# Kernel optimization log

Measured on AMD Instinct MI355X. Metric: run time of the kernel, lower is better.

Reference implementation:

```python
import jax, jax.numpy as jnp
import numpy as np

B, T = 8, 32
D = 256                      # recurrent dim = 4*8*8 (product of embed dims)
SPEAKERS = 2
OUT_CELL = 64
N_CLASSES = 6
NUM_LAYERS = 2               # original shares ONE QRNNCell across layers ([cell]*num_layers)
BETA = 0.8                   # QActivation beta (scale_factor = 1)

def _unitary(rng, n):
    a = rng.normal(size=(n, n)) + 1j * rng.normal(size=(n, n))
    q, _ = np.linalg.qr(a)
    return jnp.asarray(q.real, jnp.float32), jnp.asarray(q.imag, jnp.float32)

def setup_inputs():
    key = jax.random.key(0)
    ks = jax.random.split(key, 18)
    rng = np.random.default_rng(0)
    def lin(k, fi, fo):
        kw, kb = jax.random.split(k)
        lim = 1.0 / np.sqrt(fi)
        return (jax.random.uniform(kw, (fi, fo), jnp.float32, -lim, lim),
                jax.random.uniform(kb, (fo,), jnp.float32, -lim, lim))
    Wt, bt = lin(ks[0], 300, 4)
    Wa, ba = lin(ks[1], 74, 8)
    Wv, bv = lin(ks[2], 35, 8)
    W1, b1 = lin(ks[3], D, OUT_CELL)
    W2, b2 = lin(ks[4], OUT_CELL, N_CLASSES)
    Ux_r, Ux_i = _unitary(rng, D)
    Uh_r, Uh_i = _unitary(rng, D)
    two_pi = float(2.0 * np.pi)
    return {
        'x_text': jax.random.normal(ks[5], (B, T, 300), jnp.float32),
        'x_audio': jax.random.normal(ks[6], (B, T, 74), jnp.float32),
        'x_video': jax.random.normal(ks[7], (B, T, 35), jnp.float32),
        'smask': jax.random.uniform(ks[8], (B, T, SPEAKERS), jnp.float32),
        'Wt': Wt, 'bt': bt, 'Wa': Wa, 'ba': ba, 'Wv': Wv, 'bv': bv,
        'Pt': jax.random.uniform(ks[9], (SPEAKERS, 4), jnp.float32, 0.0, two_pi),
        'Pa': jax.random.uniform(ks[10], (SPEAKERS, 8), jnp.float32, 0.0, two_pi),
        'Pv': jax.random.uniform(ks[11], (SPEAKERS, 8), jnp.float32, 0.0, two_pi),
        'Ux_r': Ux_r, 'Ux_i': Ux_i, 'Uh_r': Uh_r, 'Uh_i': Uh_i,
        'Lambda': jax.random.normal(ks[12], (), jnp.float32),
        'Kr': jax.random.normal(ks[13], (D, D), jnp.float32),
        'Ki': jax.random.normal(ks[14], (D, D), jnp.float32),
        'W1': W1, 'b1': b1, 'W2': W2, 'b2': b2,
    }

def _forward(x_text, x_audio, x_video, spk, Wt, bt, Wa, ba, Wv, bv, Pt, Pa, Pv,
             Ux_r, Ux_i, Uh_r, Uh_i, Lambda, Kr, Ki, W1, b1, W2, b2):
    def pure_state(x, W, b, P):
        r = jax.nn.relu(x @ W + b)
        amp = r / jnp.maximum(jnp.linalg.norm(r, axis=-1, keepdims=True), 1e-12)  # F.normalize
        ph = P[spk]                                   # (B,T,e) phase lookup by speaker id
        return amp * jnp.cos(ph), amp * jnp.sin(ph)   # ComplexMultiply
    tr_, ti_ = pure_state(x_text, Wt, bt, Pt)
    ar_, ai_ = pure_state(x_audio, Wa, ba, Pa)
    vr_, vi_ = pure_state(x_video, Wv, bv, Pv)
    def ckron(xr, xi, yr, yi):                        # QProduct: complex Kronecker product
        rr = jnp.einsum('bti,btj->btij', xr, yr) - jnp.einsum('bti,btj->btij', xi, yi)
        ii = jnp.einsum('bti,btj->btij', xr, yi) + jnp.einsum('bti,btj->btij', xi, yr)
        b_, t_ = rr.shape[:2]
        return rr.reshape(b_, t_, -1), ii.reshape(b_, t_, -1)
    pr, pi = ckron(tr_, ti_, ar_, ai_)
    pr, pi = ckron(pr, pi, vr_, vi_)                  # (B,T,D)
    # QOuter: rho = |psi><psi|, stored time-major for the scan
    rho_r = jnp.einsum('bti,btj->tbij', pr, pr) + jnp.einsum('bti,btj->tbij', pi, pi)
    rho_i = jnp.einsum('bti,btj->tbij', pi, pr) - jnp.einsum('bti,btj->tbij', pr, pi)
    lam = jax.nn.sigmoid(Lambda)
    eye = jnp.eye(D, dtype=pr.dtype) / D
    def evolve(Ur, Ui, rr, ri):                       # U rho U^dagger (complex, real/imag parts)
        Ar = jnp.einsum('pq,bqr->bpr', Ur, rr) - jnp.einsum('pq,bqr->bpr', Ui, ri)
        Ai = jnp.einsum('pq,bqr->bpr', Ur, ri) + jnp.einsum('pq,bqr->bpr', Ui, rr)
        Br = jnp.einsum('bpq,rq->bpr', Ar, Ur) + jnp.einsum('bpq,rq->bpr', Ai, Ui)
        Bi = jnp.einsum('bpq,rq->bpr', Ai, Ur) - jnp.einsum('bpq,rq->bpr', Ar, Ui)
        return Br, Bi
    def step(carry, x):                               # QRNNCell; activation only on emitted state
        hr, hi = carry
        xr, xi = x
        xer, xei = evolve(Ux_r, Ux_i, xr, xi)
        her, hei = evolve(Uh_r, Uh_i, hr, hi)
        nr = lam * xer + (1.0 - lam) * her
        ni = lam * xei + (1.0 - lam) * hei
        return (nr, ni), (BETA * nr + (1.0 - BETA) * eye, BETA * ni)  # QActivation (depolarize)
    xs = (rho_r, rho_i)
    for _ in range(NUM_LAYERS):                       # same (shared) cell each layer
        init = (jnp.broadcast_to(eye, rho_r.shape[1:]), jnp.zeros(rho_r.shape[1:], pr.dtype))
        _, xs = jax.lax.scan(step, init, xs)
    hr, hi = xs                                       # (T,B,D,D)
    # QMeasurement: p_k = Re <v_k| rho |v_k>, v_k L2-normalized complex vectors
    nrm = jnp.sqrt(jnp.sum(Kr * Kr + Ki * Ki, axis=-1, keepdims=True))
    mr, mi = Kr / nrm, Ki / nrm
    Prj_r = jnp.einsum('ki,kj->kij', mr, mr) + jnp.einsum('ki,kj->kij', mi, mi)
    Prj_i = jnp.einsum('ki,kj->kij', mr, mi) - jnp.einsum('ki,kj->kij', mi, mr)
    probs = jnp.einsum('tbij,kij->tbk', hr, Prj_r) - jnp.einsum('tbij,kij->tbk', hi, Prj_i)
    h1 = jax.nn.relu(probs @ W1 + b1)                 # SimpleNet (dropout = identity at eval)
    out = jnp.tanh(h1 @ W2 + b2)                      # (T,B,C)
    return jax.nn.log_softmax(jnp.moveaxis(out, 0, 1), axis=-1)  # (B,T,C)

def reference(x_text, x_audio, x_video, smask, Wt, bt, Wa, ba, Wv, bv, Pt, Pa, Pv,
              Ux_r, Ux_i, Uh_r, Uh_i, Lambda, Kr, Ki, W1, b1, W2, b2):
    spk = jnp.argmax(smask, axis=-1)
    return _forward(x_text, x_audio, x_video, spk, Wt, bt, Wa, ba, Wv, bv, Pt, Pa, Pv,
                    Ux_r, Ux_i, Uh_r, Uh_i, Lambda, Kr, Ki, W1, b1, W2, b2)
```

## Files before the change

kernel.cpp:

```cpp
#include <hip/hip_runtime.h>

#define TT 32
#define BETA_ 0.8f

typedef __bf16 bf16_t;
typedef bf16_t bf16x8 __attribute__((ext_vector_type(8)));
typedef float f32x4 __attribute__((ext_vector_type(4)));

#define PACC_F 256
#define BF_BASE_B 263168L
#define US4 262144L
#define XU  131072L
#define XIB_E (76L * US4)

__device__ inline f32x4 MF(bf16x8 a, bf16x8 b, f32x4 c) {
    return __builtin_amdgcn_mfma_f32_16x16x32_bf16(a, b, c, 0, 0, 0);
}

__device__ inline void splitW(float vr, float vi, bf16_t* o, long idx, int full) {
    bf16_t rh = (bf16_t)vr; o[idx] = rh;
    bf16_t ih = (bf16_t)vi; o[65536L + idx] = ih;
    if (full) {
        o[2 * 65536L + idx] = (bf16_t)(vr - (float)rh);
        o[3 * 65536L + idx] = (bf16_t)(vi - (float)ih);
    }
}

__global__ __launch_bounds__(256) void k_prep(
    const float* __restrict__ xt, const float* __restrict__ xa, const float* __restrict__ xv,
    const float* __restrict__ sm,
    const float* __restrict__ Wt, const float* __restrict__ bt,
    const float* __restrict__ Wa, const float* __restrict__ ba,
    const float* __restrict__ Wv, const float* __restrict__ bv,
    const float* __restrict__ Pt, const float* __restrict__ Pa, const float* __restrict__ Pv,
    const float* __restrict__ Uxr, const float* __restrict__ Uxi,
    const float* __restrict__ Uhr, const float* __restrict__ Uhi,
    const float* __restrict__ Lam, const float* __restrict__ Kr, const float* __restrict__ Ki,
    void* wsv)
{
    float* WF = (float*)wsv;
    bf16_t* bf = (bf16_t*)((char*)wsv + BF_BASE_B);
    const int blk = blockIdx.x, tid = threadIdx.x;
    __shared__ float red[256];
    __shared__ float rt[4], ra[8], rv[8], inv3[3];

    if (blk == 0) {
        if (tid != 0) return;
        float lam = 1.f / (1.f + expf(-Lam[0]));
        float oml = 1.f - lam;
        WF[0] = lam;
        WF[1] = BETA_ * BETA_ * lam * lam;
        float w = 1.f;
        for (int n = 0; n < 64; ++n) { WF[64 + n] = w; w *= oml; }
        float a1 = 1.f / 256.f, a2 = 1.f / 256.f;
        for (int t = 0; t < 32; ++t) {
            a1 = oml * a1;
            float y1 = BETA_ * a1 + (1.f - BETA_) / 256.f;
            a2 = lam * y1 + oml * a2;
            WF[8 + t] = BETA_ * a2 + (1.f - BETA_) / 256.f;
        }
        return;
    }
    if (blk < 513) {
        int i = (blk - 1) & 255, j = tid;
        if (blk < 257) {
            splitW(Uxr[i * 256 + j], Uxi[i * 256 + j], bf + 0 * US4, (long)i * 256 + j, 1);
        } else {
            float vr = Uhr[i * 256 + j], vi = Uhi[i * 256 + j];
            splitW(vr, vi, bf + 1 * US4, (long)i * 256 + j, 1);
            splitW(vr, vi, bf + 2 * US4, (long)j * 256 + i, 1);
        }
        return;
    }
    if (blk < 769) {
        const int colS = blk - 513;
        const int t0 = colS >> 3, b = colS & 7;
        const long bt_ = (long)b * TT + t0;
        if (tid < 4) {
            float acc = bt[tid];
            const float* x = xt + bt_ * 300;
            for (int q = 0; q < 300; ++q) acc = fmaf(x[q], Wt[q * 4 + tid], acc);
            rt[tid] = fmaxf(acc, 0.f);
        } else if (tid < 12) {
            int u = tid - 4;
            float acc = ba[u];
            const float* x = xa + bt_ * 74;
            for (int q = 0; q < 74; ++q) acc = fmaf(x[q], Wa[q * 8 + u], acc);
            ra[u] = fmaxf(acc, 0.f);
        } else if (tid < 20) {
            int u = tid - 12;
            float acc = bv[u];
            const float* x = xv + bt_ * 35;
            for (int q = 0; q < 35; ++q) acc = fmaf(x[q], Wv[q * 8 + u], acc);
            rv[u] = fmaxf(acc, 0.f);
        }
        __syncthreads();
        if (tid == 0) {
            float s = 0.f; for (int u = 0; u < 4; ++u) s += rt[u] * rt[u];
            inv3[0] = 1.f / fmaxf(sqrtf(s), 1e-12f);
            s = 0.f; for (int u = 0; u < 8; ++u) s += ra[u] * ra[u];
            inv3[1] = 1.f / fmaxf(sqrtf(s), 1e-12f);
            s = 0.f; for (int u = 0; u < 8; ++u) s += rv[u] * rv[u];
            inv3[2] = 1.f / fmaxf(sqrtf(s), 1e-12f);
        }
        __syncthreads();
        float s0 = sm[bt_ * 2], s1 = sm[bt_ * 2 + 1];
        int spk = (s1 > s0) ? 1 : 0;
        int d = tid;
        int ti = d >> 6, ai = (d >> 3) & 7, vi = d & 7;
        float amp = (rt[ti] * inv3[0]) * (ra[ai] * inv3[1]) * (rv[vi] * inv3[2]);
        float ph = Pt[spk * 4 + ti] + Pa[spk * 8 + ai] + Pv[spk * 8 + vi];
        splitW(amp * cosf(ph), amp * sinf(ph), bf + 3 * US4, (long)colS * 256 + d, 1);
        return;
    }
    if (blk < 1025) {
        int k = blk - 769, i = tid;
        float vr = Kr[k * 256 + i], vi = Ki[k * 256 + i];
        red[i] = vr * vr + vi * vi;
        __syncthreads();
        for (int s = 128; s > 0; s >>= 1) { if (i < s) red[i] += red[i + s]; __syncthreads(); }
        float inv = 1.f / sqrtf(red[0]);
        splitW(vr * inv, -vi * inv, bf + 44 * US4, (long)k * 256 + i, 1);
        return;
    }
    WF[PACC_F + (blk - 1025) * 256 + tid] = 0.f;
}

template<int LO, int WFull>
__device__ __forceinline__ void chain_body(const bf16_t* __restrict__ A,
                                           const bf16_t* __restrict__ B,
                                           bf16_t* __restrict__ C,
                                           int m0, int n0, int wm, int wn, int fr, int fg)
{
    constexpr int NP = LO ? 2 : 4;
    const bf16_t* Ab = A + (long)(m0 + wm * 32 + fr) * 256 + fg * 8;
    const bf16_t* Bb = B + (long)(n0 + wn * 32 + fr) * 256 + fg * 8;
    f32x4 rp[2][2] = {}, rn[2][2] = {}, im[2][2] = {};
    bf16x8 a0[2][NP], b0[2][NP], a1[2][NP], b1[2][NP];

#define CLD(abuf, bbuf, ks)                                                            \
    {                                                                                  \
        _Pragma("unroll") for (int fm = 0; fm < 2; ++fm)                               \
            _Pragma("unroll") for (int pl = 0; pl < NP; ++pl)                          \
                abuf[fm][pl] = *(const bf16x8*)(Ab + pl * 65536L + fm * 4096L + (ks) * 32); \
        _Pragma("unroll") for (int fn = 0; fn < 2; ++fn)                               \
            _Pragma("unroll") for (int pl = 0; pl < NP; ++pl)                          \
                bbuf[fn][pl] = *(const bf16x8*)(Bb + pl * 65536L + fn * 4096L + (ks) * 32); \
    }
#define CMM(abuf, bbuf)                                                                \
    {                                                                                  \
        _Pragma("unroll") for (int fm = 0; fm < 2; ++fm)                               \
            _Pragma("unroll") for (int fn = 0; fn < 2; ++fn) {                         \
                rp[fm][fn] = MF(abuf[fm][0], bbuf[fn][0], rp[fm][fn]);                 \
                rn[fm][fn] = MF(abuf[fm][1], bbuf[fn][1], rn[fm][fn]);                 \
                im[fm][fn] = MF(abuf[fm][0], bbuf[fn][1], im[fm][fn]);                 \
                im[fm][fn] = MF(abuf[fm][1], bbuf[fn][0], im[fm][fn]);                 \
                if (!LO) {                                                             \
                    rp[fm][fn] = MF(abuf[fm][0], bbuf[fn][2], rp[fm][fn]);             \
                    rp[fm][fn] = MF(abuf[fm][2], bbuf[fn][0], rp[fm][fn]);             \
                    rn[fm][fn] = MF(abuf[fm][1], bbuf[fn][3], rn[fm][fn]);             \
                    rn[fm][fn] = MF(abuf[fm][3], bbuf[fn][1], rn[fm][fn]);             \
                    im[fm][fn] = MF(abuf[fm][0], bbuf[fn][3], im[fm][fn]);             \
                    im[fm][fn] = MF(abuf[fm][2], bbuf[fn][1], im[fm][fn]);             \
                    im[fm][fn] = MF(abuf[fm][1], bbuf[fn][2], im[fm][fn]);             \
                    im[fm][fn] = MF(abuf[fm][3], bbuf[fn][0], im[fm][fn]);             \
                }                                                                      \
            }                                                                          \
    }
    CLD(a0, b0, 0);
    CLD(a1, b1, 1);
    CMM(a0, b0); CLD(a0, b0, 2);
    CMM(a1, b1); CLD(a1, b1, 3);
    CMM(a0, b0); CLD(a0, b0, 4);
    CMM(a1, b1); CLD(a1, b1, 5);
    CMM(a0, b0); CLD(a0, b0, 6);
    CMM(a1, b1); CLD(a1, b1, 7);
    CMM(a0, b0);
    CMM(a1, b1);
#undef CLD
#undef CMM
#pragma unroll
    for (int fm = 0; fm < 2; ++fm)
#pragma unroll
        for (int fn = 0; fn < 2; ++fn)
#pragma unroll
            for (int r4 = 0; r4 < 4; ++r4) {
                int m = m0 + wm * 32 + fm * 16 + fg * 4 + r4;
                int n = n0 + wn * 32 + fn * 16 + fr;
                float vr = rp[fm][fn][r4] - rn[fm][fn][r4];
                splitW(vr, im[fm][fn][r4], C, (long)m * 256 + n, WFull);
            }
}

struct Jobs {
    long aB[4], aS[4], bB[4], cB[4], cS[4];
    int cnt[4], lo[4], wf[4];
};

__global__ __launch_bounds__(256, 2) void k_chain(void* wsv, Jobs J)
{
    bf16_t* bf = (bf16_t*)((char*)wsv + BF_BASE_B);
    int z = blockIdx.y, j = 0;
    while (z >= J.cnt[j]) { z -= J.cnt[j]; ++j; }
    const bf16_t* A = bf + J.aB[j] + (long)z * J.aS[j];
    const bf16_t* B = bf + J.bB[j];
    bf16_t*       C = bf + J.cB[j] + (long)z * J.cS[j];
    const int m0 = (blockIdx.x & 3) * 64, n0 = (blockIdx.x >> 2) * 64;
    const int tid = threadIdx.x, lane = tid & 63, w = tid >> 6;
    const int wm = w >> 1, wn = w & 1, fr = lane & 15, fg = lane >> 4;
    if (J.lo[j])      chain_body<1, 0>(A, B, C, m0, n0, wm, wn, fr, fg);
    else if (J.wf[j]) chain_body<0, 1>(A, B, C, m0, n0, wm, wn, fr, fg);
    else              chain_body<0, 0>(A, B, C, m0, n0, wm, wn, fr, fg);
}

struct MJ { int pref[33]; };

__global__ __launch_bounds__(256, 3) void k_measure7(void* wsv, MJ J)
{
    float* WF = (float*)wsv;
    bf16_t* bf = (bf16_t*)((char*)wsv + BF_BASE_B);
    int bid = blockIdx.x;
    int t = 0;
    while (bid >= J.pref[t + 1]) ++t;
    int jid = bid - J.pref[t];
    const int kblk = jid & 3;
    int g = jid >> 2;
    int c = 0;
    for (;;) { int cnt2 = ((t - c) >> 3) + 1; if (g < cnt2) break; g -= cnt2; ++c; }
    const int colc = g;
    const int k0 = kblk * 64;

    const int tid = threadIdx.x, lane = tid & 63, w = tid >> 6;
    const int wm = w >> 1, wn = w & 1;
    const int fr = lane & 15, fg = lane >> 4;
    __shared__ float part[64][9];

    int g2_[2], t0_[2], val_[2];
    const bf16_t* Bb_[2];
#pragma unroll
    for (int fn = 0; fn < 2; ++fn) {
        g2_[fn] = colc * 64 + wn * 32 + fn * 16 + fr;
        t0_[fn] = g2_[fn] >> 3;
        int av = t - c - t0_[fn];
        val_[fn] = (av >= 0);
        Bb_[fn] = bf + XIB_E + (long)(val_[fn] ? av : 0) * XU + (long)g2_[fn] * 256 + fg * 8;
    }
    const bf16_t* Ab = bf + (44L + c) * US4 + (long)(k0 + wm * 32 + fr) * 256 + fg * 8;

    f32x4 rp[2][2] = {}, rn[2][2] = {}, im[2][2] = {};
    bf16x8 a0[2][2], b0[2][2], a1[2][2], b1[2][2];

#define MLD(abuf, bbuf, ks)                                                            \
    {                                                                                  \
        _Pragma("unroll") for (int fm = 0; fm < 2; ++fm)                               \
            _Pragma("unroll") for (int pl = 0; pl < 2; ++pl)                           \
                abuf[fm][pl] = *(const bf16x8*)(Ab + pl * 65536L + fm * 4096L + (ks) * 32); \
        _Pragma("unroll") for (int fn = 0; fn < 2; ++fn)                               \
            _Pragma("unroll") for (int pl = 0; pl < 2; ++pl) {                         \
                bf16x8 v = bf16x8{};                                                   \
                if (val_[fn]) v = *(const bf16x8*)(Bb_[fn] + pl * 65536L + (ks) * 32); \
                bbuf[fn][pl] = v;                                                      \
            }                                                                          \
    }
#define MMM(abuf, bbuf)                                                                \
    {                                                                                  \
        _Pragma("unroll") for (int fm = 0; fm < 2; ++fm)                               \
            _Pragma("unroll") for (int fn = 0; fn < 2; ++fn) {                         \
                rp[fm][fn] = MF(abuf[fm][0], bbuf[fn][0], rp[fm][fn]);                 \
                rn[fm][fn] = MF(abuf[fm][1], bbuf[fn][1], rn[fm][fn]);                 \
                im[fm][fn] = MF(abuf[fm][0], bbuf[fn][1], im[fm][fn]);                 \
                im[fm][fn] = MF(abuf[fm][1], bbuf[fn][0], im[fm][fn]);                 \
            }                                                                          \
    }
    MLD(a0, b0, 0);
    MLD(a1, b1, 1);
    MMM(a0, b0); MLD(a0, b0, 2);
    MMM(a1, b1); MLD(a1, b1, 3);
    MMM(a0, b0); MLD(a0, b0, 4);
    MMM(a1, b1); MLD(a1, b1, 5);
    MMM(a0, b0); MLD(a0, b0, 6);
    MMM(a1, b1); MLD(a1, b1, 7);
    MMM(a0, b0);
    MMM(a1, b1);
#undef MLD
#undef MMM

    for (int e = tid; e < 64 * 9; e += 256) (&part[0][0])[e] = 0.f;
    __syncthreads();
#pragma unroll
    for (int fm = 0; fm < 2; ++fm)
#pragma unroll
        for (int fn = 0; fn < 2; ++fn)
#pragma unroll
            for (int r4 = 0; r4 < 4; ++r4) {
                float vr = rp[fm][fn][r4] - rn[fm][fn][r4];
                float vi = im[fm][fn][r4];
                float v = vr * vr + vi * vi;
                int kl = wm * 32 + fm * 16 + fg * 4 + r4;
                if (val_[fn] && t0_[fn] <= t)
                    atomicAdd(&part[kl][g2_[fn] & 7], WF[64 + t - t0_[fn]] * v);
            }
    __syncthreads();
    float* pacc = WF + PACC_F;
    for (int e = tid; e < 512; e += 256) {
        int kl = e >> 3, b = e & 7;
        float v = part[kl][b];
        if (v != 0.f) atomicAdd(&pacc[((t * 8 + b) << 8) + k0 + kl], v);
    }
}

__global__ __launch_bounds__(64) void k_mlp(
    const float* __restrict__ W1, const float* __restrict__ b1,
    const float* __restrict__ W2, const float* __restrict__ b2,
    const float* __restrict__ WF, float* __restrict__ out)
{
    const int t = blockIdx.x >> 3, b = blockIdx.x & 7;
    const int tid = threadIdx.x;
    __shared__ float pp[256], hh[64], oo[6];
    float ft = WF[8 + t], s2 = WF[1];
    const float* pacc = WF + PACC_F + ((t * 8 + b) << 8);
    for (int k = tid; k < 256; k += 64) pp[k] = ft + s2 * pacc[k];
    __syncthreads();
    float acc = b1[tid];
    for (int k = 0; k < 256; ++k) acc = fmaf(pp[k], W1[k * 64 + tid], acc);
    hh[tid] = fmaxf(acc, 0.f);
    __syncthreads();
    if (tid < 6) {
        float a = b2[tid];
        for (int k = 0; k < 64; ++k) a = fmaf(hh[k], W2[k * 6 + tid], a);
        oo[tid] = tanhf(a);
    }
    __syncthreads();
    if (tid == 0) {
        float m = oo[0];
        for (int c2 = 1; c2 < 6; ++c2) m = fmaxf(m, oo[c2]);
        float s = 0.f;
        for (int c2 = 0; c2 < 6; ++c2) s += expf(oo[c2] - m);
        float lse = m + logf(s);
        for (int c2 = 0; c2 < 6; ++c2) out[((long)b * 32 + t) * 6 + c2] = oo[c2] - lse;
    }
}

static inline void setJob(Jobs& J, int i, long aB, long aS, long bB, long cB, long cS,
                          int cnt, int lo, int wf)
{
    J.aB[i] = aB; J.aS[i] = aS; J.bB[i] = bB; J.cB[i] = cB; J.cS[i] = cS;
    J.cnt[i] = cnt; J.lo[i] = lo; J.wf[i] = wf;
}

extern "C" void kernel_launch(void* const* d_in, const int* in_sizes, int n_in,
                              void* d_out, int out_size, void* d_ws, size_t ws_size,
                              hipStream_t stream)
{
    const float* xt  = (const float*)d_in[0];
    const float* xa  = (const float*)d_in[1];
    const float* xv  = (const float*)d_in[2];
    const float* sm  = (const float*)d_in[3];
    const float* Wt  = (const float*)d_in[4];
    const float* bt  = (const float*)d_in[5];
    const float* Wa  = (const float*)d_in[6];
    const float* ba  = (const float*)d_in[7];
    const float* Wv  = (const float*)d_in[8];
    const float* bv  = (const float*)d_in[9];
    const float* Pt  = (const float*)d_in[10];
    const float* Pa  = (const float*)d_in[11];
    const float* Pv  = (const float*)d_in[12];
    const float* Uxr = (const float*)d_in[13];
    const float* Uxi = (const float*)d_in[14];
    const float* Uhr = (const float*)d_in[15];
    const float* Uhi = (const float*)d_in[16];
    const float* Lam = (const float*)d_in[17];
    const float* Kr  = (const float*)d_in[18];
    const float* Ki  = (const float*)d_in[19];
    const float* W1  = (const float*)d_in[20];
    const float* b1  = (const float*)d_in[21];
    const float* W2  = (const float*)d_in[22];
    const float* b2  = (const float*)d_in[23];
    float* WF  = (float*)d_ws;
    float* out = (float*)d_out;

    k_prep<<<1281, 256, 0, stream>>>(xt, xa, xv, sm, Wt, bt, Wa, ba, Wv, bv,
                                     Pt, Pa, Pv, Uxr, Uxi, Uhr, Uhi, Lam, Kr, Ki, d_ws);

    auto U = [](int u) { return (long)u * US4; };
    dim3 blk(256);
    Jobs J;

    setJob(J, 0, U(1), 0, U(2), U(4), 0, 1, 0, 1);
    setJob(J, 1, U(2), 0, U(1), U(5), 0, 1, 0, 1);
    setJob(J, 2, U(3), 0, U(0), U(12), 0, 1, 0, 1);
    setJob(J, 3, U(44), 0, U(2), U(45), 0, 1, 0, 1);
    k_chain<<<dim3(16, 4), blk, 0, stream>>>(d_ws, J);
    setJob(J, 0, U(4), 0, U(5), U(6), 0, 1, 0, 1);
    setJob(J, 1, U(5), 0, U(4), U(7), 0, 1, 0, 1);
    setJob(J, 2, U(12), 0, U(1), U(13), 0, 1, 0, 1);
    setJob(J, 3, U(44), US4, U(5), U(46), US4, 2, 0, 1);
    k_chain<<<dim3(16, 5), blk, 0, stream>>>(d_ws, J);
    setJob(J, 0, U(6), 0, U(7), U(8), 0, 1, 0, 1);
    setJob(J, 1, U(7), 0, U(6), U(9), 0, 1, 0, 1);
    setJob(J, 2, U(12), US4, U(4), U(14), US4, 2, 0, 1);
    setJob(J, 3, U(44), US4, U(7), U(48), US4, 4, 0, 1);
    k_chain<<<dim3(16, 8), blk, 0, stream>>>(d_ws, J);
    setJob(J, 0, U(8), 0, U(9), U(10), 0, 1, 0, 1);
    setJob(J, 1, U(9), 0, U(8), U(11), 0, 1, 0, 1);
    setJob(J, 2, U(12), US4, U(6), U(16), US4, 4, 0, 1);
    setJob(J, 3, U(44), US4, U(9), U(52), US4, 8, 0, 1);
    k_chain<<<dim3(16, 14), blk, 0, stream>>>(d_ws, J);
    setJob(J, 0, U(12), US4, U(8), U(20), US4, 8, 0, 1);
    setJob(J, 1, U(44), US4, U(11), U(60), US4, 16, 0, 0);
    setJob(J, 2, 0, 0, 0, 0, 0, 0, 0, 0);
    setJob(J, 3, 0, 0, 0, 0, 0, 0, 0, 0);
    k_chain<<<dim3(16, 24), blk, 0, stream>>>(d_ws, J);
    setJob(J, 0, U(12), US4, U(10), U(28), US4, 16, 0, 0);
    setJob(J, 1, U(12), US4, U(0), XIB_E, XU, 16, 1, 0);
    setJob(J, 2, 0, 0, 0, 0, 0, 0, 0, 0);
    setJob(J, 3, 0, 0, 0, 0, 0, 0, 0, 0);
    k_chain<<<dim3(16, 32), blk, 0, stream>>>(d_ws, J);
    setJob(J, 0, U(28), US4, U(0), XIB_E + 16 * XU, XU, 16, 1, 0);
    setJob(J, 1, 0, 0, 0, 0, 0, 0, 0, 0);
    setJob(J, 2, 0, 0, 0, 0, 0, 0, 0, 0);
    setJob(J, 3, 0, 0, 0, 0, 0, 0, 0, 0);
    k_chain<<<dim3(16, 16), blk, 0, stream>>>(d_ws, J);

    MJ mj;
    mj.pref[0] = 0;
    for (int t = 0; t < 32; ++t) {
        int G = 0;
        for (int c = 0; c <= t; ++c) G += ((t - c) >> 3) + 1;
        mj.pref[t + 1] = mj.pref[t] + G * 4;
    }
    k_measure7<<<dim3(mj.pref[32], 1, 1), blk, 0, stream>>>(d_ws, mj);
    k_mlp<<<256, 64, 0, stream>>>(W1, b1, W2, b2, WF, out);
}
```

Before: 386.9 us.

## Stage chain outputs through LDS for coalesced stores; reorder measure blocks and deepen prefetch

The chain GEMM epilogue now writes the real and imaginary accumulators into a shared-memory tile and re-reads them row-wise, so each thread emits 16-element vector stores instead of scattered scalar bf16 stores. The measurement kernel's block ordering is changed to group blocks by operator index c instead of time t, which may improve locality of the shared A operand. Its load pipeline is also deepened from two to three register buffers. The costs are extra LDS traffic, added barriers and higher register pressure in the measurement kernel.

New measurement: 390.1 us. About the same (+0.8%).

```diff
diff --git a/kernel.cpp b/kernel.cpp
--- a/kernel.cpp
+++ b/kernel.cpp
@@ -130,7 +130,9 @@
 __device__ __forceinline__ void chain_body(const bf16_t* __restrict__ A,
                                            const bf16_t* __restrict__ B,
                                            bf16_t* __restrict__ C,
-                                           int m0, int n0, int wm, int wn, int fr, int fg)
+                                           int m0, int n0, int tid,
+                                           int wm, int wn, int fr, int fg,
+                                           float (*sV)[65])
 {
     constexpr int NP = LO ? 2 : 4;
     const bf16_t* Ab = A + (long)(m0 + wm * 32 + fr) * 256 + fg * 8;
@@ -179,17 +181,56 @@
     CMM(a1, b1);
 #undef CLD
 #undef CMM
+    const int r = tid >> 2, sg = tid & 3;
+    const long idx = (long)(m0 + r) * 256 + n0 + sg * 16;
 #pragma unroll
     for (int fm = 0; fm < 2; ++fm)
 #pragma unroll
         for (int fn = 0; fn < 2; ++fn)
 #pragma unroll
-            for (int r4 = 0; r4 < 4; ++r4) {
-                int m = m0 + wm * 32 + fm * 16 + fg * 4 + r4;
-                int n = n0 + wn * 32 + fn * 16 + fr;
-                float vr = rp[fm][fn][r4] - rn[fm][fn][r4];
-                splitW(vr, im[fm][fn][r4], C, (long)m * 256 + n, WFull);
-            }
+            for (int r4 = 0; r4 < 4; ++r4)
+                sV[wm * 32 + fm * 16 + fg * 4 + r4][wn * 32 + fn * 16 + fr] =
+                    rp[fm][fn][r4] - rn[fm][fn][r4];
+    __syncthreads();
+    {
+        __align__(16) bf16_t hi[16], lo[16];
+#pragma unroll
+        for (int q = 0; q < 16; ++q) {
+            float v = sV[r][sg * 16 + q];
+            hi[q] = (bf16_t)v;
+            if (WFull) lo[q] = (bf16_t)(v - (float)hi[q]);
+        }
+        *(uint4*)(C + idx) = *(uint4*)(hi);
+        *(uint4*)(C + idx + 8) = *(uint4*)(hi + 8);
+        if (WFull) {
+            *(uint4*)(C + 131072L + idx) = *(uint4*)(lo);
+            *(uint4*)(C + 131072L + idx + 8) = *(uint4*)(lo + 8);
+        }
+    }
+    __syncthreads();
+#pragma unroll
+    for (int fm = 0; fm < 2; ++fm)
+#pragma unroll
+        for (int fn = 0; fn < 2; ++fn)
+#pragma unroll
+            for (int r4 = 0; r4 < 4; ++r4)
+                sV[wm * 32 + fm * 16 + fg * 4 + r4][wn * 32 + fn * 16 + fr] = im[fm][fn][r4];
+    __syncthreads();
+    {
+        __align__(16) bf16_t hi[16], lo[16];
+#pragma unroll
+        for (int q = 0; q < 16; ++q) {
+            float v = sV[r][sg * 16 + q];
+            hi[q] = (bf16_t)v;
+            if (WFull) lo[q] = (bf16_t)(v - (float)hi[q]);
+        }
+        *(uint4*)(C + 65536L + idx) = *(uint4*)(hi);
+        *(uint4*)(C + 65536L + idx + 8) = *(uint4*)(hi + 8);
+        if (WFull) {
+            *(uint4*)(C + 196608L + idx) = *(uint4*)(lo);
+            *(uint4*)(C + 196608L + idx + 8) = *(uint4*)(lo + 8);
+        }
+    }
 }
 
 struct Jobs {
@@ -200,6 +241,7 @@
 __global__ __launch_bounds__(256, 2) void k_chain(void* wsv, Jobs J)
 {
     bf16_t* bf = (bf16_t*)((char*)wsv + BF_BASE_B);
+    __shared__ float sV[64][65];
     int z = blockIdx.y, j = 0;
     while (z >= J.cnt[j]) { z -= J.cnt[j]; ++j; }
     const bf16_t* A = bf + J.aB[j] + (long)z * J.aS[j];
@@ -208,26 +250,26 @@
     const int m0 = (blockIdx.x & 3) * 64, n0 = (blockIdx.x >> 2) * 64;
     const int tid = threadIdx.x, lane = tid & 63, w = tid >> 6;
     const int wm = w >> 1, wn = w & 1, fr = lane & 15, fg = lane >> 4;
-    if (J.lo[j])      chain_body<1, 0>(A, B, C, m0, n0, wm, wn, fr, fg);
-    else if (J.wf[j]) chain_body<0, 1>(A, B, C, m0, n0, wm, wn, fr, fg);
-    else              chain_body<0, 0>(A, B, C, m0, n0, wm, wn, fr, fg);
+    if (J.lo[j])      chain_body<1, 0>(A, B, C, m0, n0, tid, wm, wn, fr, fg, sV);
+    else if (J.wf[j]) chain_body<0, 1>(A, B, C, m0, n0, tid, wm, wn, fr, fg, sV);
+    else              chain_body<0, 0>(A, B, C, m0, n0, tid, wm, wn, fr, fg, sV);
 }
 
 struct MJ { int pref[33]; };
 
-__global__ __launch_bounds__(256, 3) void k_measure7(void* wsv, MJ J)
+__global__ __launch_bounds__(256, 3) void k_measure8(void* wsv, MJ J)
 {
     float* WF = (float*)wsv;
     bf16_t* bf = (bf16_t*)((char*)wsv + BF_BASE_B);
     int bid = blockIdx.x;
-    int t = 0;
-    while (bid >= J.pref[t + 1]) ++t;
-    int jid = bid - J.pref[t];
-    const int kblk = jid & 3;
-    int g = jid >> 2;
     int c = 0;
-    for (;;) { int cnt2 = ((t - c) >> 3) + 1; if (g < cnt2) break; g -= cnt2; ++c; }
-    const int colc = g;
+    while (bid >= J.pref[c + 1]) ++c;
+    int rem = bid - J.pref[c];
+    const int kblk = rem & 3;
+    int g = rem >> 2;
+    int m = 0;
+    for (;;) { int cnt2 = (m >> 3) + 1; if (g < cnt2) break; g -= cnt2; ++m; }
+    const int t = c + m, colc = g;
     const int k0 = kblk * 64;
 
     const int tid = threadIdx.x, lane = tid & 63, w = tid >> 6;
@@ -241,14 +283,14 @@
     for (int fn = 0; fn < 2; ++fn) {
         g2_[fn] = colc * 64 + wn * 32 + fn * 16 + fr;
         t0_[fn] = g2_[fn] >> 3;
-        int av = t - c - t0_[fn];
+        int av = m - t0_[fn];
         val_[fn] = (av >= 0);
         Bb_[fn] = bf + XIB_E + (long)(val_[fn] ? av : 0) * XU + (long)g2_[fn] * 256 + fg * 8;
     }
     const bf16_t* Ab = bf + (44L + c) * US4 + (long)(k0 + wm * 32 + fr) * 256 + fg * 8;
 
     f32x4 rp[2][2] = {}, rn[2][2] = {}, im[2][2] = {};
-    bf16x8 a0[2][2], b0[2][2], a1[2][2], b1[2][2];
+    bf16x8 a0[2][2], b0[2][2], a1[2][2], b1[2][2], a2[2][2], b2[2][2];
 
 #define MLD(abuf, bbuf, ks)                                                            \
     {                                                                                  \
@@ -274,12 +316,13 @@
     }
     MLD(a0, b0, 0);
     MLD(a1, b1, 1);
-    MMM(a0, b0); MLD(a0, b0, 2);
-    MMM(a1, b1); MLD(a1, b1, 3);
-    MMM(a0, b0); MLD(a0, b0, 4);
-    MMM(a1, b1); MLD(a1, b1, 5);
+    MLD(a2, b2, 2);
+    MMM(a0, b0); MLD(a0, b0, 3);
+    MMM(a1, b1); MLD(a1, b1, 4);
+    MMM(a2, b2); MLD(a2, b2, 5);
     MMM(a0, b0); MLD(a0, b0, 6);
     MMM(a1, b1); MLD(a1, b1, 7);
+    MMM(a2, b2);
     MMM(a0, b0);
     MMM(a1, b1);
 #undef MLD
@@ -424,11 +467,11 @@
 
     MJ mj;
     mj.pref[0] = 0;
-    for (int t = 0; t < 32; ++t) {
+    for (int c = 0; c < 32; ++c) {
         int G = 0;
-        for (int c = 0; c <= t; ++c) G += ((t - c) >> 3) + 1;
-        mj.pref[t + 1] = mj.pref[t] + G * 4;
-    }
-    k_measure7<<<dim3(mj.pref[32], 1, 1), blk, 0, stream>>>(d_ws, mj);
+        for (int m = 0; m <= 31 - c; ++m) G += (m >> 3) + 1;
+        mj.pref[c + 1] = mj.pref[c] + G * 4;
+    }
+    k_measure8<<<dim3(mj.pref[32], 1, 1), blk, 0, stream>>>(d_ws, mj);
     k_mlp<<<256, 64, 0, stream>>>(W1, b1, W2, b2, WF, out);
 }
```
